# Performance work log

Measured on AMD Instinct MI355X. Metric: run time of the kernel, lower is better.

## Reference

```python
import jax, jax.numpy as jnp
import numpy as np
from jax import lax

B, T, D_LAT, D, H, J = 2048, 60, 100, 512, 256, 6
LRELU_SLOPE = 0.2
BN_EPS = 1e-5

# --- fixed kinematic-chain constants (stand-in for URDF: 6-DoF right arm) ---
AXES = np.array([[0,0,1],[1,0,0],[0,1,0],[1,0,0],[0,1,0],[1,0,0]], np.float32)
OFFS = np.array([[0,0,0.10],[0,0,0],[0,0,0],[0,-0.25,0],[0,0,0],[0,-0.25,0]], np.float32)
LOWER = np.array([-3.1416,-1.5708,-3.1416,-2.6,-1.5708,-1.2], np.float32)
UPPER = np.array([ 3.1416, 1.5708, 3.1416, 0.1, 1.5708, 1.2], np.float32)
FING1 = np.array([0.0,-0.08, 0.02], np.float32)
FING4 = np.array([0.0,-0.08,-0.02], np.float32)

def _skew(a):
    return np.array([[0,-a[2],a[1]],[a[2],0,-a[0]],[-a[1],a[0],0]], np.float32)

def fk_batch(joints):
    """joints: [B,T,6] normalized in [0,1]-ish -> poses [B,T,3,3]."""
    th = joints * (UPPER - LOWER) + LOWER                      # denormalize
    bt = th.shape[:2]
    R = jnp.broadcast_to(jnp.eye(3, dtype=th.dtype), bt + (3, 3))
    p = jnp.zeros(bt + (3,), th.dtype)
    pos = []
    for j in range(J):
        K = jnp.asarray(_skew(AXES[j]))
        a = th[..., j][..., None, None]
        Rj = jnp.eye(3, dtype=th.dtype) + jnp.sin(a) * K + (1.0 - jnp.cos(a)) * (K @ K)
        p = p + jnp.einsum('btij,j->bti', R, jnp.asarray(OFFS[j]))  # Trans then Rot
        R = jnp.einsum('btij,btjk->btik', R, Rj)
        pos.append(p)
    shoulder2, forearm, wrist = pos[1], pos[3], pos[5]
    f1 = wrist + jnp.einsum('btij,j->bti', R, jnp.asarray(FING1))
    f4 = wrist + jnp.einsum('btij,j->bti', R, jnp.asarray(FING4))
    body_L = (jnp.linalg.norm(shoulder2 - forearm, axis=-1)
              + jnp.linalg.norm(wrist - forearm, axis=-1)) * 0.5   # [B,T]
    rel = jnp.stack([wrist - shoulder2, f1 - shoulder2, f4 - shoulder2], axis=2)
    return rel / body_L[..., None, None]

def gru_dir(x, Wih, Whh, bih, bhh, reverse):
    xg = jnp.einsum('btd,gd->btg', x, Wih) + bih               # [B,T,3H]
    xg = jnp.swapaxes(xg, 0, 1)                                 # [T,B,3H]
    def step(h, g):
        gh = h @ Whh.T + bhh
        r = jax.nn.sigmoid(g[:, :H] + gh[:, :H])
        zz = jax.nn.sigmoid(g[:, H:2*H] + gh[:, H:2*H])
        n = jnp.tanh(g[:, 2*H:] + r * gh[:, 2*H:])
        hn = (1.0 - zz) * n + zz * h
        return hn, hn
    h0 = jnp.zeros((x.shape[0], H), x.dtype)
    _, ys = lax.scan(step, h0, xg, reverse=reverse)
    return jnp.swapaxes(ys, 0, 1)                               # [B,T,H]

def setup_inputs() -> dict:
    key = jax.random.key(0)
    ks = jax.random.split(key, 12)
    s = 0.05
    inp = {
        'z': jax.random.normal(ks[0], (B, D_LAT), jnp.float32),
        'W_fc': jax.random.normal(ks[1], (D, D_LAT), jnp.float32) * s,
        'b_fc': jnp.zeros((D,), jnp.float32),
        'bn_g': jnp.ones((D,), jnp.float32),
        'bn_b': jnp.zeros((D,), jnp.float32),
        'Wih_f': jax.random.normal(ks[2], (3*H, D), jnp.float32) * s,
        'Whh_f': jax.random.normal(ks[3], (3*H, H), jnp.float32) * s,
        'bih_f': jnp.zeros((3*H,), jnp.float32),
        'bhh_f': jnp.zeros((3*H,), jnp.float32),
        'Wih_b': jax.random.normal(ks[4], (3*H, D), jnp.float32) * s,
        'Whh_b': jax.random.normal(ks[5], (3*H, H), jnp.float32) * s,
        'bih_b': jnp.zeros((3*H,), jnp.float32),
        'bhh_b': jnp.zeros((3*H,), jnp.float32),
        'attn_W1': jax.random.normal(ks[6], (H, 2*H), jnp.float32) * s,
        'attn_b1': jnp.zeros((H,), jnp.float32),
        'attn_W2': jax.random.normal(ks[7], (H,), jnp.float32) * s,
        'joint_W': jax.random.normal(ks[8], (J, 2*H), jnp.float32) * s,
        'joint_b': jnp.zeros((J,), jnp.float32),
    }
    return inp

def reference(z, W_fc, b_fc, bn_g, bn_b, Wih_f, Whh_f, bih_f, bhh_f,
              Wih_b, Whh_b, bih_b, bhh_b, attn_W1, attn_b1, attn_W2,
              joint_W, joint_b):
    # fc: Linear + BatchNorm1d (training-mode batch stats) + LeakyReLU(0.2)
    h0 = z @ W_fc.T + b_fc                                      # [B,512]
    mu = jnp.mean(h0, axis=0)
    var = jnp.mean((h0 - mu) ** 2, axis=0)
    hb = (h0 - mu) * jax.lax.rsqrt(var + BN_EPS) * bn_g + bn_b
    h = jnp.where(hb >= 0, hb, LRELU_SLOPE * hb)
    x = jnp.broadcast_to(h[:, None, :], (h.shape[0], T, D))     # repeat over seq
    # bidirectional GRU
    gf = gru_dir(x, Wih_f, Whh_f, bih_f, bhh_f, False)
    gb = gru_dir(x, Wih_b, Whh_b, bih_b, bhh_b, True)
    gru_out = jnp.concatenate([gf, gb], axis=-1)                # [B,T,512]
    # attention over time
    a = jnp.tanh(jnp.einsum('btd,hd->bth', gru_out, attn_W1) + attn_b1)
    w = jax.nn.softmax(jnp.einsum('bth,h->bt', a, attn_W2), axis=1)[..., None]
    c = jnp.sum(w * gru_out, axis=1, keepdims=True)             # [B,1,512]
    joints = jnp.einsum('btd,jd->btj', gru_out + c, joint_W) + joint_b
    return fk_batch(joints)                                     # [B,T,3,3]
```

## Files before the change

### kernel.cpp

```cpp
#include <hip/hip_runtime.h>
#include <hip/hip_fp16.h>

#define NB 2048
#define NT 60
#define NDL 100
#define ND 512
#define NH 256
#define NG 768

#define L2E  1.44269504f
#define L2E2 2.88539008f

typedef const float* __restrict__ fpp;
typedef _Float16 half8 __attribute__((ext_vector_type(8)));
typedef float floatx4 __attribute__((ext_vector_type(4)));

__device__ __forceinline__ float fast_rcp(float x) {
  return __builtin_amdgcn_rcpf(x);
}
__device__ __forceinline__ float fast_exp2(float x) {
#if __has_builtin(__builtin_amdgcn_exp2f)
  return __builtin_amdgcn_exp2f(x);
#else
  return exp2f(x);
#endif
}
__device__ __forceinline__ float fsin(float x) {
#if __has_builtin(__builtin_amdgcn_sinf)
  return __builtin_amdgcn_sinf(x * 0.15915494309189535f);
#else
  return __sinf(x);
#endif
}
__device__ __forceinline__ float fcos(float x) {
#if __has_builtin(__builtin_amdgcn_cosf)
  return __builtin_amdgcn_cosf(x * 0.15915494309189535f);
#else
  return __cosf(x);
#endif
}

__global__ __launch_bounds__(256) void gemm_fc(
    fpp A, fpp Bm, fpp bias, float* __restrict__ C,
    int M, int N, int K, int lda, int ldb, int ldc)
{
  __shared__ float As[16][68];
  __shared__ float Bs[16][68];
  const int bm = blockIdx.x * 64, bn = blockIdx.y * 64;
  const int tid = threadIdx.x;
  const int tx = tid & 15, ty = tid >> 4;
  float acc[4][4] = {};
  for (int k0 = 0; k0 < K; k0 += 16) {
#pragma unroll
    for (int i = 0; i < 4; i++) {
      int e = tid + i * 256;
      int m = e >> 4, k = e & 15;
      As[k][m] = (k0 + k < K) ? A[(size_t)(bm + m) * lda + k0 + k] : 0.f;
      Bs[k][m] = (k0 + k < K) ? Bm[(size_t)(bn + m) * ldb + k0 + k] : 0.f;
    }
    __syncthreads();
#pragma unroll
    for (int kk = 0; kk < 16; kk++) {
      float4 av = *(const float4*)&As[kk][ty * 4];
      float4 bv = *(const float4*)&Bs[kk][tx * 4];
      float a_[4] = {av.x, av.y, av.z, av.w};
      float b_[4] = {bv.x, bv.y, bv.z, bv.w};
#pragma unroll
      for (int i = 0; i < 4; i++)
#pragma unroll
        for (int j = 0; j < 4; j++)
          acc[i][j] = fmaf(a_[i], b_[j], acc[i][j]);
    }
    __syncthreads();
  }
#pragma unroll
  for (int i = 0; i < 4; i++) {
    int m = bm + ty * 4 + i;
#pragma unroll
    for (int j = 0; j < 4; j++) {
      int n = bn + tx * 4 + j;
      C[(size_t)m * ldc + n] = acc[i][j] + bias[n];
    }
  }
}

__global__ __launch_bounds__(256) void bn_partial(
    const float* __restrict__ h0, float* __restrict__ s1g,
    float* __restrict__ s2g)
{
  const int r0 = blockIdx.x * 32;
  const int tid = threadIdx.x;
  float a1 = 0.f, a2 = 0.f, b1 = 0.f, b2 = 0.f;
  for (int r = 0; r < 32; r++) {
    float v = h0[(size_t)(r0 + r) * ND + tid];
    float w = h0[(size_t)(r0 + r) * ND + tid + 256];
    a1 += v; a2 += v * v;
    b1 += w; b2 += w * w;
  }
  atomicAdd(&s1g[tid], a1);
  atomicAdd(&s2g[tid], a2);
  atomicAdd(&s1g[tid + 256], b1);
  atomicAdd(&s2g[tid + 256], b2);
}

__global__ void bn_lrelu_h16(const float* __restrict__ h0,
                             fpp g, fpp b,
                             const float* __restrict__ s1g,
                             const float* __restrict__ s2g,
                             __half* __restrict__ h16g)
{
  int idx = blockIdx.x * 256 + threadIdx.x;
  int d = idx & (ND - 1);
  float mu = s1g[d] * (1.f / NB);
  float var = s2g[d] * (1.f / NB) - mu * mu;
  float sc = g[d] * rsqrtf(var + 1e-5f);
  float sh = b[d] - mu * sc;
  float v = h0[idx] * sc + sh;
  h16g[idx] = __float2half(v >= 0.f ? v : 0.2f * v);
}

__global__ void convert_w(fpp whf, fpp whb, fpp w1, fpp wif, fpp wib, fpp jw,
                          __half* __restrict__ o_whf, __half* __restrict__ o_whb,
                          __half* __restrict__ o_w1, __half* __restrict__ o_wif,
                          __half* __restrict__ o_wib, __half* __restrict__ o_jw)
{
  int idx = blockIdx.x * 256 + threadIdx.x;
  if (idx < 196608) {
    float s = ((idx >> 16) == 2) ? L2E2 : L2E;
    o_whf[idx] = __float2half(whf[idx] * s);
  } else if (idx < 393216) {
    int e = idx - 196608;
    float s = ((e >> 16) == 2) ? L2E2 : L2E;
    o_whb[e] = __float2half(whb[e] * s);
  } else if (idx < 524288) {
    int e = idx - 393216;
    o_w1[e] = __float2half(w1[e] * L2E2);
  } else if (idx < 917504) {
    int e = idx - 524288;
    float s = ((e >> 17) == 2) ? L2E2 : L2E;
    o_wif[e] = __float2half(wif[e] * s);
  } else if (idx < 1310720) {
    int e = idx - 917504;
    float s = ((e >> 17) == 2) ? L2E2 : L2E;
    o_wib[e] = __float2half(wib[e] * s);
  } else if (idx < 1318912) {
    int e = idx - 1310720;
    o_jw[e] = (e < 6 * ND) ? __float2half(jw[e]) : __float2half(0.f);
  }
}

__global__ __launch_bounds__(256) void gemm16_dual(
    const __half* __restrict__ A,
    const __half* __restrict__ B0, const __half* __restrict__ B1,
    fpp bias0, fpp bias1, float* __restrict__ C0, float* __restrict__ C1,
    int N, int K)
{
  const __half* __restrict__ Bm = blockIdx.z ? B1 : B0;
  fpp bias = blockIdx.z ? bias1 : bias0;
  float* __restrict__ C = blockIdx.z ? C1 : C0;

  __shared__ __half As[64 * 40];
  __shared__ __half Bs[64 * 40];
  const int bm = blockIdx.x * 64, bn = blockIdx.y * 64;
  const int tid = threadIdx.x;
  const int wave = tid >> 6, lane = tid & 63;
  const int lm = lane & 15, quad = lane >> 4;
  floatx4 acc[4];
#pragma unroll
  for (int nt = 0; nt < 4; nt++) acc[nt] = (floatx4){0.f, 0.f, 0.f, 0.f};

  const int row = tid >> 2, kc = tid & 3;
  for (int k0 = 0; k0 < K; k0 += 32) {
    __syncthreads();
    *(float4*)&As[row * 40 + kc * 8] =
      *(const float4*)&A[(size_t)(bm + row) * K + k0 + kc * 8];
    *(float4*)&Bs[row * 40 + kc * 8] =
      *(const float4*)&Bm[(size_t)(bn + row) * K + k0 + kc * 8];
    __syncthreads();
    half8 af = *(const half8*)&As[(wave * 16 + lm) * 40 + quad * 8];
#pragma unroll
    for (int nt = 0; nt < 4; nt++) {
      half8 bf = *(const half8*)&Bs[(nt * 16 + lm) * 40 + quad * 8];
      acc[nt] = __builtin_amdgcn_mfma_f32_16x16x32_f16(af, bf, acc[nt], 0, 0, 0);
    }
  }
#pragma unroll
  for (int nt = 0; nt < 4; nt++) {
    int n = bn + nt * 16 + lm;
    float bv = bias[n] * ((n < 2 * NH) ? L2E : L2E2);
#pragma unroll
    for (int r = 0; r < 4; r++) {
      int m = bm + wave * 16 + quad * 4 + r;
      C[(size_t)m * N + n] = acc[nt][r] + bv;
    }
  }
}

#define GATES(C) do {                                                        \
    _Pragma("unroll")                                                        \
    for (int r = 0; r < 4; r++) {                                            \
      float er = fast_exp2(-acc[0][C][r]);                                   \
      float rg = fast_rcp(1.f + er);                                         \
      float ez = fast_exp2(-acc[1][C][r]);                                   \
      float tt = fast_exp2(fmaf(rg, acc[2][C][r], xn4[C][r]));               \
      float dd = tt + 1.f;                                                   \
      float num = fmaf(tt, ez + hp[C][r], hp[C][r] - ez);                    \
      float den = fmaf(dd, ez, dd);                                          \
      float hv = num * fast_rcp(den);                                        \
      hp[C][r] = hv;                                                         \
      hCur[(quad * 4 + r) * 264 + (n0 + C * 16 + lm)] = __float2half(hv);    \
    }                                                                        \
  } while (0)

#define CHAIN(C) do {                                                        \
    half8 t6[3], t7[3];                                                      \
    _Pragma("unroll")                                                        \
    for (int g = 0; g < 3; g++) {                                            \
      const __half* wp = &wts[wb + (g * 4 + C * 2) * 512];                   \
      t6[g] = *(const half8*)wp;                                             \
      t7[g] = *(const half8*)(wp + 512);                                     \
    }                                                                        \
    _Pragma("unroll")                                                        \
    for (int kb = 0; kb < 6; kb++)                                           \
      _Pragma("unroll")                                                      \
      for (int g = 0; g < 3; g++)                                            \
        acc[g][C] = __builtin_amdgcn_mfma_f32_16x16x32_f16(                  \
            a[kb], __builtin_bit_cast(half8, breg[g][C][kb]), acc[g][C],     \
            0, 0, 0);                                                        \
    _Pragma("unroll")                                                        \
    for (int g = 0; g < 3; g++)                                              \
      acc[g][C] = __builtin_amdgcn_mfma_f32_16x16x32_f16(                    \
          a[6], t6[g], acc[g][C], 0, 0, 0);                                  \
    _Pragma("unroll")                                                        \
    for (int g = 0; g < 3; g++)                                              \
      acc[g][C] = __builtin_amdgcn_mfma_f32_16x16x32_f16(                    \
          a[7], t7[g], acc[g][C], 0, 0, 0);                                  \
  } while (0)

__global__ __launch_bounds__(512, 2) void gru_persistent(
    const float* __restrict__ xg_f, const float* __restrict__ xg_b,
    const __half* __restrict__ whh16_f, const __half* __restrict__ whh16_b,
    fpp bhh_f, fpp bhh_b, __half* __restrict__ seq)
{
  const int dir  = blockIdx.x & 1;
  const int tile = blockIdx.x >> 1;
  const int bm   = tile * 16;
  const float* __restrict__ xg = dir ? xg_b : xg_f;
  const __half* __restrict__ Whh = dir ? whh16_b : whh16_f;
  fpp bhh = dir ? bhh_b : bhh_f;
  const int dcol = dir * NH;
  const int tid = threadIdx.x;
  const int wave = tid >> 6, lane = tid & 63;
  const int lm = lane & 15, quad = lane >> 4;
  const int n0 = wave * 32;

  __shared__ __half h16s[2][16 * 264];
  __shared__ __half wts[96 * 512];

  floatx4 breg[3][2][6];
  {
    const __half* bp[3][2];
#pragma unroll
    for (int g = 0; g < 3; g++)
#pragma unroll
      for (int c = 0; c < 2; c++)
        bp[g][c] = Whh + (size_t)(g * NH + n0 + c * 16 + lm) * NH + quad * 8;

#pragma unroll
    for (int g = 0; g < 3; g++)
#pragma unroll
      for (int c = 0; c < 2; c++)
#pragma unroll
        for (int kb = 0; kb < 6; kb++)
          breg[g][c][kb] = *(const floatx4*)(bp[g][c] + kb * 32);
#pragma unroll
    for (int g = 0; g < 3; g++)
#pragma unroll
      for (int c = 0; c < 2; c++)
#pragma unroll
        for (int kb = 0; kb < 6; kb++)
          asm volatile("" : "+v"(breg[g][c][kb]));

#pragma unroll
    for (int g = 0; g < 3; g++)
#pragma unroll
      for (int c = 0; c < 2; c++)
#pragma unroll
        for (int k2 = 0; k2 < 2; k2++)
          *(float4*)&wts[(wave * 12 + g * 4 + c * 2 + k2) * 512 + lane * 8] =
            *(const float4*)(bp[g][c] + 192 + k2 * 32);
  }

  floatx4 xr4[2], xz4[2], xn4[2];
  float bn_[2];
#pragma unroll
  for (int c = 0; c < 2; c++) {
    int n = n0 + c * 16 + lm;
    float br = bhh[n] * L2E, bz = bhh[NH + n] * L2E;
    bn_[c] = bhh[2 * NH + n] * L2E2;
#pragma unroll
    for (int r = 0; r < 4; r++) {
      int m = bm + quad * 4 + r;
      const float* xp = xg + (size_t)m * NG + n;
      xr4[c][r] = xp[0] + br;
      xz4[c][r] = xp[NH] + bz;
      xn4[c][r] = xp[2 * NH];
    }
  }

  float hp[2][4];
#pragma unroll
  for (int c = 0; c < 2; c++)
#pragma unroll
    for (int r = 0; r < 4; r++) hp[c][r] = 0.f;

  const int arow = lm * 264 + quad * 8;
  const int cm = tid >> 5, cpart = tid & 31;
  const int wb = wave * 6144 + lane * 8;

  __half* seqp = seq + ((size_t)(bm + cm) * NT + (dir ? NT - 1 : 0)) * ND
                 + dcol + cpart * 8;
  const ptrdiff_t seqd = dir ? -(ptrdiff_t)ND : (ptrdiff_t)ND;

  for (int step = 0; step < NT; step++) {
    const int cur = step & 1, prv = cur ^ 1;
    __half* __restrict__ hCur = h16s[cur];
    const __half* __restrict__ hPrv = h16s[prv];
    floatx4 acc[3][2];
#pragma unroll
    for (int c = 0; c < 2; c++) {
      acc[0][c] = xr4[c];
      acc[1][c] = xz4[c];
      acc[2][c] = (floatx4){bn_[c], bn_[c], bn_[c], bn_[c]};
    }

    if (step > 0) {
      {
        float4 v = *(const float4*)&hPrv[cm * 264 + cpart * 8];
        *(float4*)seqp = v;
        seqp += seqd;
      }
      half8 a[8];
#pragma unroll
      for (int kb = 0; kb < 8; kb++)
        a[kb] = *(const half8*)&hPrv[arow + kb * 32];

      __builtin_amdgcn_s_setprio(1);
      CHAIN(0);
      __builtin_amdgcn_s_setprio(0);
      GATES(0);
      __builtin_amdgcn_s_setprio(1);
      CHAIN(1);
      __builtin_amdgcn_s_setprio(0);
      GATES(1);
    } else {
      GATES(0);
      GATES(1);
    }
    __syncthreads();
  }

  {
    const __half* hLast = h16s[(NT - 1) & 1];
    float4 v = *(const float4*)&hLast[cm * 264 + cpart * 8];
    *(float4*)seqp = v;
  }
}

__global__ __launch_bounds__(512, 4) void attn_score_mfma(
    const __half* __restrict__ seq, const __half* __restrict__ w116,
    const __half* __restrict__ jw16, fpp b1, fpp W2,
    float* __restrict__ scores, float* __restrict__ gJ)
{
  const int bm = blockIdx.x * 128;
  const int tid = threadIdx.x;
  const int wave = tid >> 6, lane = tid & 63;
  const int lm = lane & 15, quad = lane >> 4;
  const int mh = wave & 1;
  const int nh = wave >> 1;

  __shared__ __half As[128 * 40];
  __shared__ __half Bs[256 * 40];
  __shared__ __half Js[16 * 40];
  __shared__ float partial[4][128];

  floatx4 acc[4][4];
  floatx4 accJ[4];
#pragma unroll
  for (int t = 0; t < 4; t++) {
#pragma unroll
    for (int u = 0; u < 4; u++) acc[t][u] = (floatx4){0.f, 0.f, 0.f, 0.f};
    accJ[t] = (floatx4){0.f, 0.f, 0.f, 0.f};
  }

  const int srow = tid >> 2, skc8 = (tid & 3) * 8;

  for (int k0 = 0; k0 < ND; k0 += 32) {
    __syncthreads();
    *(float4*)&As[srow * 40 + skc8] =
      *(const float4*)&seq[(size_t)(bm + srow) * ND + k0 + skc8];
#pragma unroll
    for (int i = 0; i < 2; i++)
      *(float4*)&Bs[(srow + i * 128) * 40 + skc8] =
        *(const float4*)&w116[(size_t)(srow + i * 128) * ND + k0 + skc8];
    if (tid < 64)
      *(float4*)&Js[srow * 40 + skc8] =
        *(const float4*)&jw16[(size_t)srow * ND + k0 + skc8];
    __syncthreads();

    half8 a[4];
#pragma unroll
    for (int t = 0; t < 4; t++)
      a[t] = *(const half8*)&As[((mh * 4 + t) * 16 + lm) * 40 + quad * 8];
#pragma unroll
    for (int u = 0; u < 4; u++) {
      half8 bf = *(const half8*)&Bs[((nh * 4 + u) * 16 + lm) * 40 + quad * 8];
#pragma unroll
      for (int t = 0; t < 4; t++)
        acc[t][u] = __builtin_amdgcn_mfma_f32_16x16x32_f16(a[t], bf, acc[t][u], 0, 0, 0);
    }
    if (nh == 3) {
      half8 bj = *(const half8*)&Js[lm * 40 + quad * 8];
#pragma unroll
      for (int t = 0; t < 4; t++)
        accJ[t] = __builtin_amdgcn_mfma_f32_16x16x32_f16(a[t], bj, accJ[t], 0, 0, 0);
    }
  }

  float rs[4][4] = {};
#pragma unroll
  for (int u = 0; u < 4; u++) {
    int n = (nh * 4 + u) * 16 + lm;
    float b1v = b1[n] * L2E2, w2v = W2[n];
#pragma unroll
    for (int t = 0; t < 4; t++)
#pragma unroll
      for (int r = 0; r < 4; r++) {
        float tt = fast_exp2(acc[t][u][r] + b1v);
        float th = fmaf(-2.f, fast_rcp(tt + 1.f), 1.f);
        rs[t][r] = fmaf(th, w2v, rs[t][r]);
      }
  }
#pragma unroll
  for (int t = 0; t < 4; t++)
#pragma unroll
    for (int r = 0; r < 4; r++) {
      rs[t][r] += __shfl_xor(rs[t][r], 1);
      rs[t][r] += __shfl_xor(rs[t][r], 2);
      rs[t][r] += __shfl_xor(rs[t][r], 4);
      rs[t][r] += __shfl_xor(rs[t][r], 8);
    }
  if (lm == 0) {
#pragma unroll
    for (int t = 0; t < 4; t++)
#pragma unroll
      for (int r = 0; r < 4; r++)
        partial[nh][mh * 64 + t * 16 + quad * 4 + r] = rs[t][r];
  }
  if (nh == 3) {
#pragma unroll
    for (int t = 0; t < 4; t++)
#pragma unroll
      for (int r = 0; r < 4; r++) {
        int row = bm + mh * 64 + t * 16 + quad * 4 + r;
        gJ[(size_t)row * 16 + lm] = accJ[t][r];
      }
  }
  __syncthreads();
  if (tid < 128)
    scores[bm + tid] = partial[0][tid] + partial[1][tid] +
                       partial[2][tid] + partial[3][tid];
}

__constant__ float c_lower[6] = {-3.1416f, -1.5708f, -3.1416f, -2.6f, -1.5708f, -1.2f};
__constant__ float c_upper[6] = { 3.1416f,  1.5708f,  3.1416f,  0.1f,  1.5708f,  1.2f};

__global__ __launch_bounds__(64) void attn_post(
    const float* __restrict__ scores_in, const float* __restrict__ gJ,
    fpp jb, float* __restrict__ out)
{
  const int b = blockIdx.x;
  const int t = threadIdx.x;

  float v = (t < NT) ? scores_in[(size_t)b * NT + t] : -1e30f;
  float m = v;
#pragma unroll
  for (int off = 32; off >= 1; off >>= 1) m = fmaxf(m, __shfl_xor(m, off));
  float e = (t < NT) ? __expf(v - m) : 0.f;
  float sum = e;
#pragma unroll
  for (int off = 32; off >= 1; off >>= 1) sum += __shfl_xor(sum, off);
  float w = e * fast_rcp(sum);

  __shared__ float gj[NT * 16];
  __shared__ float wl[64];
  __shared__ float cj[16];
  wl[t] = w;
  const float* gsrc = gJ + (size_t)b * NT * 16;
#pragma unroll
  for (int i = 0; i < 15; i++) gj[t + i * 64] = gsrc[t + i * 64];
  __syncthreads();

  if (t < 16) {
    float s = 0.f;
    for (int tt = 0; tt < NT; tt++) s += wl[tt] * gj[tt * 16 + t];
    cj[t] = s;
  }
  __syncthreads();

  if (t >= NT) return;

  float th[6];
#pragma unroll
  for (int j = 0; j < 6; j++) {
    float jnt = gj[t * 16 + j] + cj[j] + jb[j];
    th[j] = jnt * (c_upper[j] - c_lower[j]) + c_lower[j];
  }

  float c0x = 1.f, c0y = 0.f, c0z = 0.f;
  float c1x = 0.f, c1y = 1.f, c1z = 0.f;
  float c2x = 0.f, c2y = 0.f, c2z = 1.f;
  float px = 0.f, py = 0.f, pz = 0.1f;
  float s, cc, tx_, ty_, tz_, ux_, uy_, uz_;

  s = fsin(th[0]); cc = fcos(th[0]);
  tx_ = cc * c0x + s * c1x; ty_ = cc * c0y + s * c1y; tz_ = cc * c0z + s * c1z;
  ux_ = -s * c0x + cc * c1x; uy_ = -s * c0y + cc * c1y; uz_ = -s * c0z + cc * c1z;
  c0x = tx_; c0y = ty_; c0z = tz_; c1x = ux_; c1y = uy_; c1z = uz_;

  float shx = px, shy = py, shz = pz;
  s = fsin(th[1]); cc = fcos(th[1]);
  tx_ = cc * c1x + s * c2x; ty_ = cc * c1y + s * c2y; tz_ = cc * c1z + s * c2z;
  ux_ = -s * c1x + cc * c2x; uy_ = -s * c1y + cc * c2y; uz_ = -s * c1z + cc * c2z;
  c1x = tx_; c1y = ty_; c1z = tz_; c2x = ux_; c2y = uy_; c2z = uz_;

  s = fsin(th[2]); cc = fcos(th[2]);
  tx_ = cc * c0x - s * c2x; ty_ = cc * c0y - s * c2y; tz_ = cc * c0z - s * c2z;
  ux_ = s * c0x + cc * c2x; uy_ = s * c0y + cc * c2y; uz_ = s * c0z + cc * c2z;
  c0x = tx_; c0y = ty_; c0z = tz_; c2x = ux_; c2y = uy_; c2z = uz_;

  px -= 0.25f * c1x; py -= 0.25f * c1y; pz -= 0.25f * c1z;
  float fox = px, foy = py, foz = pz;
  s = fsin(th[3]); cc = fcos(th[3]);
  tx_ = cc * c1x + s * c2x; ty_ = cc * c1y + s * c2y; tz_ = cc * c1z + s * c2z;
  ux_ = -s * c1x + cc * c2x; uy_ = -s * c1y + cc * c2y; uz_ = -s * c1z + cc * c2z;
  c1x = tx_; c1y = ty_; c1z = tz_; c2x = ux_; c2y = uy_; c2z = uz_;

  s = fsin(th[4]); cc = fcos(th[4]);
  tx_ = cc * c0x - s * c2x; ty_ = cc * c0y - s * c2y; tz_ = cc * c0z - s * c2z;
  ux_ = s * c0x + cc * c2x; uy_ = s * c0y + cc * c2y; uz_ = s * c0z + cc * c2z;
  c0x = tx_; c0y = ty_; c0z = tz_; c2x = ux_; c2y = uy_; c2z = uz_;

  px -= 0.25f * c1x; py -= 0.25f * c1y; pz -= 0.25f * c1z;
  float wx = px, wy = py, wz = pz;
  s = fsin(th[5]); cc = fcos(th[5]);
  tx_ = cc * c1x + s * c2x; ty_ = cc * c1y + s * c2y; tz_ = cc * c1z + s * c2z;
  ux_ = -s * c1x + cc * c2x; uy_ = -s * c1y + cc * c2y; uz_ = -s * c1z + cc * c2z;
  c1x = tx_; c1y = ty_; c1z = tz_; c2x = ux_; c2y = uy_; c2z = uz_;

  float f1x = wx - 0.08f * c1x + 0.02f * c2x;
  float f1y = wy - 0.08f * c1y + 0.02f * c2y;
  float f1z = wz - 0.08f * c1z + 0.02f * c2z;
  float f4x = wx - 0.08f * c1x - 0.02f * c2x;
  float f4y = wy - 0.08f * c1y - 0.02f * c2y;
  float f4z = wz - 0.08f * c1z - 0.02f * c2z;

  float dsx = shx - fox, dsy = shy - foy, dsz = shz - foz;
  float dwx = wx - fox, dwy = wy - foy, dwz = wz - foz;
  float bodyL = 0.5f * (sqrtf(dsx * dsx + dsy * dsy + dsz * dsz) +
                        sqrtf(dwx * dwx + dwy * dwy + dwz * dwz));
  float inv = fast_rcp(bodyL);

  float* o = out + ((size_t)b * NT + t) * 9;
  o[0] = (wx - shx) * inv; o[1] = (wy - shy) * inv; o[2] = (wz - shz) * inv;
  o[3] = (f1x - shx) * inv; o[4] = (f1y - shy) * inv; o[5] = (f1z - shz) * inv;
  o[6] = (f4x - shx) * inv; o[7] = (f4y - shy) * inv; o[8] = (f4z - shz) * inv;
}

extern "C" void kernel_launch(void* const* d_in, const int* in_sizes, int n_in,
                              void* d_out, int out_size, void* d_ws, size_t ws_size,
                              hipStream_t stream)
{
  fpp z     = (fpp)d_in[0];
  fpp W_fc  = (fpp)d_in[1];
  fpp b_fc  = (fpp)d_in[2];
  fpp bn_g  = (fpp)d_in[3];
  fpp bn_b  = (fpp)d_in[4];
  fpp Wih_f = (fpp)d_in[5];
  fpp Whh_f = (fpp)d_in[6];
  fpp bih_f = (fpp)d_in[7];
  fpp bhh_f = (fpp)d_in[8];
  fpp Wih_b = (fpp)d_in[9];
  fpp Whh_b = (fpp)d_in[10];
  fpp bih_b = (fpp)d_in[11];
  fpp bhh_b = (fpp)d_in[12];
  fpp aW1   = (fpp)d_in[13];
  fpp ab1   = (fpp)d_in[14];
  fpp aW2   = (fpp)d_in[15];
  fpp jW    = (fpp)d_in[16];
  fpp jb    = (fpp)d_in[17];

  float* ws     = (float*)d_ws;
  float* h0     = ws;
  float* xg_f   = h0 + 1048576;
  float* xg_b   = xg_f + 1572864;
  float* bns1   = xg_b + 1572864;
  float* bns2   = bns1 + 512;
  float* scores = bns2 + 512;
  float* cbuf   = scores + 122880;
  __half* gseq    = (__half*)(cbuf + 1048576);
  __half* whh16_f = gseq + 62914560;
  __half* whh16_b = whh16_f + 196608;
  __half* w116    = whh16_b + 196608;
  __half* wih16_f = w116 + 131072;
  __half* wih16_b = wih16_f + 393216;
  __half* h16g    = wih16_b + 393216;
  __half* jw16    = h16g + 1048576;
  float*  gJ      = (float*)(jw16 + 8192);

  convert_w<<<5152, 256, 0, stream>>>(Whh_f, Whh_b, aW1, Wih_f, Wih_b, jW,
                                      whh16_f, whh16_b, w116, wih16_f, wih16_b,
                                      jw16);
  hipMemsetAsync(bns1, 0, 1024 * sizeof(float), stream);
  gemm_fc<<<dim3(32, 8), 256, 0, stream>>>(z, W_fc, b_fc, h0,
                                           NB, ND, NDL, NDL, NDL, ND);
  bn_partial<<<64, 256, 0, stream>>>(h0, bns1, bns2);
  bn_lrelu_h16<<<4096, 256, 0, stream>>>(h0, bn_g, bn_b, bns1, bns2, h16g);
  gemm16_dual<<<dim3(32, 12, 2), 256, 0, stream>>>(
      h16g, wih16_f, wih16_b, bih_f, bih_b, xg_f, xg_b, NG, ND);
  gru_persistent<<<256, 512, 0, stream>>>(xg_f, xg_b, whh16_f, whh16_b,
                                          bhh_f, bhh_b, gseq);
  attn_score_mfma<<<960, 512, 0, stream>>>(gseq, w116, jw16, ab1, aW2,
                                           scores, gJ);
  attn_post<<<NB, 64, 0, stream>>>(scores, gJ, jb, (float*)d_out);
}
```

Baseline: 282.4 us.

## Split GRU recurrence across 16 waves with all Whh weights in registers

The persistent GRU kernel now runs 1024 threads per block instead of 512, so each wave owns 16 hidden columns instead of 32. This lets every wave hold its full recurrent weight slice in registers (3x8 fragments) and drops the shared-memory weight spill and its per-step LDS reads. Each step becomes a single 24-MFMA chain per wave followed by the gate math, giving more wave-level parallelism per step. The cost is fewer registers per thread under the new launch bounds and a __syncthreads across twice as many waves. Separately, the BN partial-sum kernel uses 8 rows per block over 256 blocks instead of 32 rows over 64, which adds more atomics.

After: 549.9 us. +94.7%, slower.

```diff
diff --git a/kernel.cpp b/kernel.cpp
--- a/kernel.cpp
+++ b/kernel.cpp
@@ -88,10 +88,10 @@
     const float* __restrict__ h0, float* __restrict__ s1g,
     float* __restrict__ s2g)
 {
-  const int r0 = blockIdx.x * 32;
+  const int r0 = blockIdx.x * 8;
   const int tid = threadIdx.x;
   float a1 = 0.f, a2 = 0.f, b1 = 0.f, b2 = 0.f;
-  for (int r = 0; r < 32; r++) {
+  for (int r = 0; r < 8; r++) {
     float v = h0[(size_t)(r0 + r) * ND + tid];
     float w = h0[(size_t)(r0 + r) * ND + tid + 256];
     a1 += v; a2 += v * v;
@@ -196,48 +196,7 @@
   }
 }
 
-#define GATES(C) do {                                                        \
-    _Pragma("unroll")                                                        \
-    for (int r = 0; r < 4; r++) {                                            \
-      float er = fast_exp2(-acc[0][C][r]);                                   \
-      float rg = fast_rcp(1.f + er);                                         \
-      float ez = fast_exp2(-acc[1][C][r]);                                   \
-      float tt = fast_exp2(fmaf(rg, acc[2][C][r], xn4[C][r]));               \
-      float dd = tt + 1.f;                                                   \
-      float num = fmaf(tt, ez + hp[C][r], hp[C][r] - ez);                    \
-      float den = fmaf(dd, ez, dd);                                          \
-      float hv = num * fast_rcp(den);                                        \
-      hp[C][r] = hv;                                                         \
-      hCur[(quad * 4 + r) * 264 + (n0 + C * 16 + lm)] = __float2half(hv);    \
-    }                                                                        \
-  } while (0)
-
-#define CHAIN(C) do {                                                        \
-    half8 t6[3], t7[3];                                                      \
-    _Pragma("unroll")                                                        \
-    for (int g = 0; g < 3; g++) {                                            \
-      const __half* wp = &wts[wb + (g * 4 + C * 2) * 512];                   \
-      t6[g] = *(const half8*)wp;                                             \
-      t7[g] = *(const half8*)(wp + 512);                                     \
-    }                                                                        \
-    _Pragma("unroll")                                                        \
-    for (int kb = 0; kb < 6; kb++)                                           \
-      _Pragma("unroll")                                                      \
-      for (int g = 0; g < 3; g++)                                            \
-        acc[g][C] = __builtin_amdgcn_mfma_f32_16x16x32_f16(                  \
-            a[kb], __builtin_bit_cast(half8, breg[g][C][kb]), acc[g][C],     \
-            0, 0, 0);                                                        \
-    _Pragma("unroll")                                                        \
-    for (int g = 0; g < 3; g++)                                              \
-      acc[g][C] = __builtin_amdgcn_mfma_f32_16x16x32_f16(                    \
-          a[6], t6[g], acc[g][C], 0, 0, 0);                                  \
-    _Pragma("unroll")                                                        \
-    for (int g = 0; g < 3; g++)                                              \
-      acc[g][C] = __builtin_amdgcn_mfma_f32_16x16x32_f16(                    \
-          a[7], t7[g], acc[g][C], 0, 0, 0);                                  \
-  } while (0)
-
-__global__ __launch_bounds__(512, 2) void gru_persistent(
+__global__ __launch_bounds__(1024, 4) void gru_persistent(
     const float* __restrict__ xg_f, const float* __restrict__ xg_b,
     const __half* __restrict__ whh16_f, const __half* __restrict__ whh16_b,
     fpp bhh_f, fpp bhh_b, __half* __restrict__ seq)
@@ -252,92 +211,61 @@
   const int tid = threadIdx.x;
   const int wave = tid >> 6, lane = tid & 63;
   const int lm = lane & 15, quad = lane >> 4;
-  const int n0 = wave * 32;
+  const int n0 = wave * 16;
 
   __shared__ __half h16s[2][16 * 264];
-  __shared__ __half wts[96 * 512];
-
-  floatx4 breg[3][2][6];
+
+  floatx4 breg[3][8];
   {
-    const __half* bp[3][2];
+#pragma unroll
+    for (int g = 0; g < 3; g++) {
+      const __half* bp = Whh + (size_t)(g * NH + n0 + lm) * NH + quad * 8;
+#pragma unroll
+      for (int kb = 0; kb < 8; kb++)
+        breg[g][kb] = *(const floatx4*)(bp + kb * 32);
+    }
 #pragma unroll
     for (int g = 0; g < 3; g++)
 #pragma unroll
-      for (int c = 0; c < 2; c++)
-        bp[g][c] = Whh + (size_t)(g * NH + n0 + c * 16 + lm) * NH + quad * 8;
-
-#pragma unroll
-    for (int g = 0; g < 3; g++)
-#pragma unroll
-      for (int c = 0; c < 2; c++)
-#pragma unroll
-        for (int kb = 0; kb < 6; kb++)
-          breg[g][c][kb] = *(const floatx4*)(bp[g][c] + kb * 32);
-#pragma unroll
-    for (int g = 0; g < 3; g++)
-#pragma unroll
-      for (int c = 0; c < 2; c++)
-#pragma unroll
-        for (int kb = 0; kb < 6; kb++)
-          asm volatile("" : "+v"(breg[g][c][kb]));
-
-#pragma unroll
-    for (int g = 0; g < 3; g++)
-#pragma unroll
-      for (int c = 0; c < 2; c++)
-#pragma unroll
-        for (int k2 = 0; k2 < 2; k2++)
-          *(float4*)&wts[(wave * 12 + g * 4 + c * 2 + k2) * 512 + lane * 8] =
-            *(const float4*)(bp[g][c] + 192 + k2 * 32);
-  }
-
-  floatx4 xr4[2], xz4[2], xn4[2];
-  float bn_[2];
-#pragma unroll
-  for (int c = 0; c < 2; c++) {
-    int n = n0 + c * 16 + lm;
+      for (int kb = 0; kb < 8; kb++)
+        asm volatile("" : "+v"(breg[g][kb]));
+  }
+
+  floatx4 xr4, xz4, xn4;
+  float bnv;
+  {
+    int n = n0 + lm;
     float br = bhh[n] * L2E, bz = bhh[NH + n] * L2E;
-    bn_[c] = bhh[2 * NH + n] * L2E2;
+    bnv = bhh[2 * NH + n] * L2E2;
 #pragma unroll
     for (int r = 0; r < 4; r++) {
       int m = bm + quad * 4 + r;
       const float* xp = xg + (size_t)m * NG + n;
-      xr4[c][r] = xp[0] + br;
-      xz4[c][r] = xp[NH] + bz;
-      xn4[c][r] = xp[2 * NH];
-    }
-  }
-
-  float hp[2][4];
-#pragma unroll
-  for (int c = 0; c < 2; c++)
-#pragma unroll
-    for (int r = 0; r < 4; r++) hp[c][r] = 0.f;
+      xr4[r] = xp[0] + br;
+      xz4[r] = xp[NH] + bz;
+      xn4[r] = xp[2 * NH];
+    }
+  }
+
+  floatx4 hp = (floatx4){0.f, 0.f, 0.f, 0.f};
 
   const int arow = lm * 264 + quad * 8;
-  const int cm = tid >> 5, cpart = tid & 31;
-  const int wb = wave * 6144 + lane * 8;
-
+  const int cm = wave, cpart = lane;
   __half* seqp = seq + ((size_t)(bm + cm) * NT + (dir ? NT - 1 : 0)) * ND
-                 + dcol + cpart * 8;
+                 + dcol + cpart * 4;
   const ptrdiff_t seqd = dir ? -(ptrdiff_t)ND : (ptrdiff_t)ND;
 
   for (int step = 0; step < NT; step++) {
     const int cur = step & 1, prv = cur ^ 1;
     __half* __restrict__ hCur = h16s[cur];
     const __half* __restrict__ hPrv = h16s[prv];
-    floatx4 acc[3][2];
-#pragma unroll
-    for (int c = 0; c < 2; c++) {
-      acc[0][c] = xr4[c];
-      acc[1][c] = xz4[c];
-      acc[2][c] = (floatx4){bn_[c], bn_[c], bn_[c], bn_[c]};
-    }
+    floatx4 acc0 = xr4, acc1 = xz4;
+    floatx4 acc2 = (floatx4){bnv, bnv, bnv, bnv};
 
     if (step > 0) {
       {
-        float4 v = *(const float4*)&hPrv[cm * 264 + cpart * 8];
-        *(float4*)seqp = v;
+        float2 v = *(const float2*)&hPrv[cm * 264 + cpart * 4];
+        *(float2*)seqp = v;
         seqp += seqd;
       }
       half8 a[8];
@@ -346,24 +274,38 @@
         a[kb] = *(const half8*)&hPrv[arow + kb * 32];
 
       __builtin_amdgcn_s_setprio(1);
-      CHAIN(0);
+#pragma unroll
+      for (int kb = 0; kb < 8; kb++) {
+        acc0 = __builtin_amdgcn_mfma_f32_16x16x32_f16(
+            a[kb], __builtin_bit_cast(half8, breg[0][kb]), acc0, 0, 0, 0);
+        acc1 = __builtin_amdgcn_mfma_f32_16x16x32_f16(
+            a[kb], __builtin_bit_cast(half8, breg[1][kb]), acc1, 0, 0, 0);
+        acc2 = __builtin_amdgcn_mfma_f32_16x16x32_f16(
+            a[kb], __builtin_bit_cast(half8, breg[2][kb]), acc2, 0, 0, 0);
+      }
       __builtin_amdgcn_s_setprio(0);
-      GATES(0);
-      __builtin_amdgcn_s_setprio(1);
-      CHAIN(1);
-      __builtin_amdgcn_s_setprio(0);
-      GATES(1);
-    } else {
-      GATES(0);
-      GATES(1);
+    }
+
+#pragma unroll
+    for (int r = 0; r < 4; r++) {
+      float er = fast_exp2(-acc0[r]);
+      float rg = fast_rcp(1.f + er);
+      float ez = fast_exp2(-acc1[r]);
+      float tt = fast_exp2(fmaf(rg, acc2[r], xn4[r]));
+      float dd = tt + 1.f;
+      float num = fmaf(tt, ez + hp[r], hp[r] - ez);
+      float den = fmaf(dd, ez, dd);
+      float hv = num * fast_rcp(den);
+      hp[r] = hv;
+      hCur[(quad * 4 + r) * 264 + n0 + lm] = __float2half(hv);
     }
     __syncthreads();
   }
 
   {
     const __half* hLast = h16s[(NT - 1) & 1];
-    float4 v = *(const float4*)&hLast[cm * 264 + cpart * 8];
-    *(float4*)seqp = v;
+    float2 v = *(const float2*)&hLast[cm * 264 + cpart * 4];
+    *(float2*)seqp = v;
   }
 }
 
@@ -624,12 +566,12 @@
   hipMemsetAsync(bns1, 0, 1024 * sizeof(float), stream);
   gemm_fc<<<dim3(32, 8), 256, 0, stream>>>(z, W_fc, b_fc, h0,
                                            NB, ND, NDL, NDL, NDL, ND);
-  bn_partial<<<64, 256, 0, stream>>>(h0, bns1, bns2);
+  bn_partial<<<256, 256, 0, stream>>>(h0, bns1, bns2);
   bn_lrelu_h16<<<4096, 256, 0, stream>>>(h0, bn_g, bn_b, bns1, bns2, h16g);
   gemm16_dual<<<dim3(32, 12, 2), 256, 0, stream>>>(
       h16g, wih16_f, wih16_b, bih_f, bih_b, xg_f, xg_b, NG, ND);
-  gru_persistent<<<256, 512, 0, stream>>>(xg_f, xg_b, whh16_f, whh16_b,
-                                          bhh_f, bhh_b, gseq);
+  gru_persistent<<<256, 1024, 0, stream>>>(xg_f, xg_b, whh16_f, whh16_b,
+                                           bhh_f, bhh_b, gseq);
   attn_score_mfma<<<960, 512, 0, stream>>>(gseq, w116, jw16, ab1, aW2,
                                            scores, gJ);
   attn_post<<<NB, 64, 0, stream>>>(scores, gJ, jb, (float*)d_out);
```
